# Performance work log

Hardware: AMD Instinct MI355X
Metric: run time of the kernel (lower is better)

Reference implementation:

```python
import jax, jax.numpy as jnp
import numpy as np

B, S = 32, 4096
HID, MEM, ATT = 512, 512, 512


def setup_inputs() -> dict:
    key = jax.random.key(0)
    k1, k2, k3, k4, k5, k6, k7 = jax.random.split(key, 7)
    scale_h = 1.0 / np.sqrt(HID)
    scale_m = 1.0 / np.sqrt(MEM)
    scale_a = 1.0 / np.sqrt(ATT)
    return {
        "hidden": jax.random.normal(k1, (B, HID), dtype=jnp.float32),
        "memory": jax.random.normal(k2, (B, S, MEM), dtype=jnp.float32),
        "mem_pad": jnp.zeros((B, S), dtype=jnp.bool_),
        "coverage": jax.random.uniform(k3, (B, S), dtype=jnp.float32),
        # params stored as (in, out) so x @ W == torch Linear(x)
        "W_h": jax.random.uniform(k4, (HID, ATT), minval=-scale_h, maxval=scale_h, dtype=jnp.float32),
        "W_m": jax.random.uniform(k5, (MEM, ATT), minval=-scale_m, maxval=scale_m, dtype=jnp.float32),
        "W_c": jax.random.uniform(k6, (ATT,), minval=-1.0, maxval=1.0, dtype=jnp.float32),
        "v": jax.random.uniform(k7, (ATT,), minval=-scale_a, maxval=scale_a, dtype=jnp.float32),
    }


def reference(hidden, memory, mem_pad, coverage, W_h, W_m, W_c, v):
    h = hidden @ W_h                                   # (B, A)
    m = jnp.einsum('bsd,da->bsa', memory, W_m)         # (B, S, A)
    c_feat = coverage[..., None] * W_c                 # (B, S, A) ; Linear(1->A) == scalar * weight row
    score = jnp.einsum('bsa,a->bs', jnp.tanh(h[:, None, :] + m + c_feat), v)  # (B, S)
    score = jnp.where(mem_pad, -jnp.inf, score)
    attn_weights = jax.nn.softmax(score, axis=-1)      # (B, S)
    context = jnp.einsum('bs,bsd->bd', attn_weights, memory)  # (B, D)
    return context, attn_weights
```

## Files before the change

### kernel.cpp

```cpp
#include <hip/hip_runtime.h>
#include <hip/hip_bf16.h>
#include <math.h>

#define BB 32
#define SS 4096
#define DMEM 512
#define DATT 512

typedef short short8 __attribute__((ext_vector_type(8)));
typedef float floatx4 __attribute__((ext_vector_type(4)));

__device__ inline short f2bf(float x) {
    unsigned u = __float_as_uint(x);
    unsigned r = (u + 0x7fffu + ((u >> 16) & 1u)) >> 16;
    return (short)(r & 0xffffu);
}

__device__ inline float fast_tanh(float x) {
    float e = __expf(2.0f * x);
    float r = __builtin_amdgcn_rcpf(e + 1.0f);
    return __builtin_fmaf(-2.0f, r, 1.0f);
}


__global__ void prep_wt_kernel(const float* __restrict__ Wm, short* __restrict__ Wt) {
    const int n0 = blockIdx.x * 32;
    const int k0 = blockIdx.y * 32;
    const int t = threadIdx.x;
    const int r = t >> 5, c = t & 31;
    __shared__ float lds[32 * 33];
#pragma unroll
    for (int j = 0; j < 4; ++j) {
        int kk = r + j * 8;
        lds[kk * 33 + c] = Wm[(size_t)(k0 + kk) * 512 + n0 + c];
    }
    __syncthreads();
#pragma unroll
    for (int j = 0; j < 4; ++j) {
        int nn = r + j * 8;
        Wt[(size_t)(n0 + nn) * 512 + k0 + c] = f2bf(lds[c * 33 + nn]);
    }
}

__global__ void prep_h_kernel(const float* __restrict__ hidden, const float* __restrict__ Wh,
                              float* __restrict__ h) {
    const int b = blockIdx.x;
    const int n = blockIdx.y * 256 + threadIdx.x;
    const int kc = blockIdx.z;
    float acc = 0.f;
#pragma unroll 8
    for (int k = kc * 128; k < kc * 128 + 128; ++k)
        acc += hidden[b * 512 + k] * Wh[(size_t)k * 512 + n];
    atomicAdd(&h[b * 512 + n], acc);
}


__global__ __launch_bounds__(1024, 4)
void fused_kernel(const float* __restrict__ memory,
                  const float* __restrict__ coverage,
                  const unsigned char* __restrict__ pad,
                  const short* __restrict__ Wt,
                  const float* __restrict__ h,
                  const float* __restrict__ Wc,
                  const float* __restrict__ v,
                  float* __restrict__ pOut,
                  float* __restrict__ mWS,
                  float* __restrict__ lWS,
                  float* __restrict__ ctxPart) {
    const int blk = blockIdx.x;
    const int b = blk >> 5;
    const int st = blk & 31;
    const int s0 = st * 128;

    const int tid = threadIdx.x;
    const int lane = tid & 63;
    const int wave = tid >> 6;
    const int wm = wave & 1;
    const int wn = wave >> 1;
    const int col = lane & 15;
    const int q = lane >> 4;

    __shared__ __align__(16) char smem[22024];
    char* bufA0 = smem;
    char* bufA1 = smem + 8192;
    float* covS   = (float*)(smem + 16384);
    float* sred   = (float*)(smem + 16896);
    float* scoreS = (float*)(smem + 20992);
    float* pS     = (float*)(smem + 21504);
    float* mlS    = (float*)(smem + 22016);
    float4* red4  = (float4*)smem;

    if (tid < 128) covS[tid] = coverage[(size_t)b * SS + s0 + tid];

    const float4* gA4 = (const float4*)(memory + ((size_t)b * SS + s0) * 512);
    const char* gB = (const char*)Wt;

    const int arow = tid >> 3, al8 = tid & 7;
    const int aoff = arow * 64 + (((al8 >> 1) ^ ((arow >> 1) & 3)) << 4) + ((al8 & 1) << 3);
    const int boff0 = (wn * 64 + col) * 1024 + q * 16;

    float4 apfA;

    floatx4 acc[4][4];
#pragma unroll
    for (int mi = 0; mi < 4; ++mi)
#pragma unroll
        for (int ni = 0; ni < 4; ++ni)
            acc[mi][ni] = (floatx4){0.f, 0.f, 0.f, 0.f};

    apfA = gA4[(size_t)arow * 128 + al8];
    {
        union { __hip_bfloat162 h2; unsigned u; } p0, p1;
        p0.h2 = __float22bfloat162_rn(make_float2(apfA.x, apfA.y));
        p1.h2 = __float22bfloat162_rn(make_float2(apfA.z, apfA.w));
        uint2 w; w.x = p0.u; w.y = p1.u;
        *(uint2*)(bufA0 + aoff) = w;
    }
    apfA = gA4[(size_t)arow * 128 + 8 + al8];
    asm volatile("s_waitcnt lgkmcnt(0)" ::: "memory");
    __builtin_amdgcn_sched_barrier(0);
    __builtin_amdgcn_s_barrier();

#pragma unroll
    for (int kt = 0; kt < 16; ++kt) {
        short8 bfc[4];
#pragma unroll
        for (int ni = 0; ni < 4; ++ni)
            bfc[ni] = *(const short8*)(gB + (size_t)(boff0 + ni * 16384) + kt * 64);

        if (kt < 15) {
            union { __hip_bfloat162 h2; unsigned u; } p0, p1;
            p0.h2 = __float22bfloat162_rn(make_float2(apfA.x, apfA.y));
            p1.h2 = __float22bfloat162_rn(make_float2(apfA.z, apfA.w));
            uint2 w; w.x = p0.u; w.y = p1.u;
            char* dst = ((kt + 1) & 1) ? bufA1 : bufA0;
            *(uint2*)(dst + aoff) = w;
            if (kt < 14)
                apfA = gA4[(size_t)arow * 128 + (kt + 2) * 8 + al8];
        }

        const char* abase = (kt & 1) ? bufA1 : bufA0;
        short8 af[4];
#pragma unroll
        for (int mi = 0; mi < 4; ++mi) {
            int row = wm * 64 + mi * 16 + col;
            af[mi] = *(const short8*)(abase + row * 64 + ((q ^ ((row >> 1) & 3)) << 4));
        }
#pragma unroll
        for (int mi = 0; mi < 4; ++mi)
#pragma unroll
            for (int ni = 0; ni < 4; ++ni)
                acc[mi][ni] = __builtin_amdgcn_mfma_f32_16x16x32_bf16(af[mi], bfc[ni], acc[mi][ni], 0, 0, 0);

        asm volatile("s_waitcnt lgkmcnt(0)" ::: "memory");
        __builtin_amdgcn_sched_barrier(0);
        __builtin_amdgcn_s_barrier();
    }

    __syncthreads();

    float hv[4], wcv[4], vv[4];
#pragma unroll
    for (int ni = 0; ni < 4; ++ni) {
        int n = wn * 64 + ni * 16 + col;
        hv[ni] = h[b * 512 + n];
        wcv[ni] = Wc[n];
        vv[ni] = v[n];
    }
    float rowAcc[4][4];
#pragma unroll
    for (int mi = 0; mi < 4; ++mi)
#pragma unroll
        for (int r = 0; r < 4; ++r)
            rowAcc[mi][r] = 0.f;
#pragma unroll
    for (int mi = 0; mi < 4; ++mi) {
#pragma unroll
        for (int r = 0; r < 4; ++r) {
            float cv = covS[wm * 64 + mi * 16 + q * 4 + r];
#pragma unroll
            for (int ni = 0; ni < 4; ++ni) {
                float val = acc[mi][ni][r] + hv[ni] + cv * wcv[ni];
                rowAcc[mi][r] += fast_tanh(val) * vv[ni];
            }
        }
    }
#pragma unroll
    for (int off = 1; off < 16; off <<= 1)
#pragma unroll
        for (int mi = 0; mi < 4; ++mi)
#pragma unroll
            for (int r = 0; r < 4; ++r)
                rowAcc[mi][r] += __shfl_xor(rowAcc[mi][r], off, 64);

    if (col == 0) {
#pragma unroll
        for (int mi = 0; mi < 4; ++mi)
#pragma unroll
            for (int r = 0; r < 4; ++r)
                sred[wn * 128 + wm * 64 + mi * 16 + q * 4 + r] = rowAcc[mi][r];
    }
    __syncthreads();

    if (tid < 128) {
        float sc = 0.f;
#pragma unroll
        for (int w = 0; w < 8; ++w) sc += sred[w * 128 + tid];
        if (pad[(size_t)b * SS + s0 + tid]) sc = -INFINITY;
        scoreS[tid] = sc;
    }
    __syncthreads();
    if (tid < 64) {
        float mx = fmaxf(scoreS[tid], scoreS[tid + 64]);
#pragma unroll
        for (int off = 32; off >= 1; off >>= 1) mx = fmaxf(mx, __shfl_xor(mx, off, 64));
        if (tid == 0) mlS[0] = mx;
    }
    __syncthreads();
    const float mtile = mlS[0];
    if (tid < 128) pS[tid] = __expf(scoreS[tid] - mtile);
    __syncthreads();
    if (tid < 64) {
        float sm = pS[tid] + pS[tid + 64];
#pragma unroll
        for (int off = 32; off >= 1; off >>= 1) sm += __shfl_xor(sm, off, 64);
        if (tid == 0) mlS[1] = sm;
    }
    __syncthreads();

    if (tid < 128) pOut[(size_t)b * SS + s0 + tid] = pS[tid];
    if (tid == 0) {
        mWS[b * 32 + st] = mtile;
        lWS[b * 32 + st] = mlS[1];
    }

    const int sg = tid >> 7;
    const int dc = tid & 127;
    const float4* m4 = (const float4*)(memory + ((size_t)b * SS + s0) * 512);
    float4 a4 = {0.f, 0.f, 0.f, 0.f};
#pragma unroll 8
    for (int i = 0; i < 16; ++i) {
        int s = sg * 16 + i;
        float w = pS[s];
        float4 f = m4[(size_t)s * 128 + dc];
        a4.x += w * f.x; a4.y += w * f.y; a4.z += w * f.z; a4.w += w * f.w;
    }
    red4[sg * 128 + dc] = a4;
    __syncthreads();
    if (tid < 128) {
        float4 o = {0.f, 0.f, 0.f, 0.f};
#pragma unroll
        for (int g2 = 0; g2 < 8; ++g2) {
            float4 r = red4[g2 * 128 + tid];
            o.x += r.x; o.y += r.y; o.z += r.z; o.w += r.w;
        }
        ((float4*)(ctxPart + ((size_t)(b * 32 + st)) * 512))[tid] = o;
    }
}

__global__ __launch_bounds__(512)
void combine_kernel(const float* __restrict__ mWS,
                    const float* __restrict__ lWS,
                    const float* __restrict__ ctxPart,
                    float* __restrict__ ctx,
                    float* __restrict__ attn) {
    const int b = blockIdx.x;
    const int tid = threadIdx.x;
    __shared__ float scaleS[32];
    __shared__ float gS[2];

    if (tid < 64) {
        float mv = (tid < 32) ? mWS[b * 32 + tid] : -INFINITY;
#pragma unroll
        for (int off = 32; off >= 1; off >>= 1) mv = fmaxf(mv, __shfl_xor(mv, off, 64));
        if (tid == 0) gS[0] = mv;
    }
    __syncthreads();
    const float gmax = gS[0];
    if (tid < 64) {
        float sc = 0.f, lv = 0.f;
        if (tid < 32) {
            sc = __expf(mWS[b * 32 + tid] - gmax);
            scaleS[tid] = sc;
            lv = lWS[b * 32 + tid] * sc;
        }
#pragma unroll
        for (int off = 32; off >= 1; off >>= 1) lv += __shfl_xor(lv, off, 64);
        if (tid == 0) gS[1] = lv;
    }
    __syncthreads();
    const float inv = 1.0f / gS[1];

    float facc = 0.f;
#pragma unroll 8
    for (int st = 0; st < 32; ++st)
        facc += ctxPart[((size_t)(b * 32 + st)) * 512 + tid] * scaleS[st];
    ctx[b * 512 + tid] = facc * inv;

#pragma unroll
    for (int j = 0; j < 8; ++j) {
        size_t idx = (size_t)b * SS + j * 512 + tid;
        attn[idx] = attn[idx] * scaleS[(j * 512 + tid) >> 7] * inv;
    }
}

extern "C" void kernel_launch(void* const* d_in, const int* in_sizes, int n_in,
                              void* d_out, int out_size, void* d_ws, size_t ws_size,
                              hipStream_t stream) {
    (void)in_sizes; (void)n_in; (void)out_size; (void)ws_size;
    const float* hidden   = (const float*)d_in[0];
    const float* memory   = (const float*)d_in[1];
    const unsigned char* mem_pad = (const unsigned char*)d_in[2];
    const float* coverage = (const float*)d_in[3];
    const float* Wh       = (const float*)d_in[4];
    const float* Wm       = (const float*)d_in[5];
    const float* Wc       = (const float*)d_in[6];
    const float* v        = (const float*)d_in[7];

    char* ws = (char*)d_ws;
    short* Wt      = (short*)ws;
    float* h       = (float*)(ws + 512 * 1024);
    float* mWS     = (float*)(ws + 576 * 1024);
    float* lWS     = (float*)(ws + 580 * 1024);
    float* ctxPart = (float*)(ws + 584 * 1024);

    float* ctx  = (float*)d_out;
    float* attn = (float*)d_out + BB * 512;

    hipMemsetAsync(h, 0, BB * 512 * sizeof(float), stream);
    prep_wt_kernel<<<dim3(16, 16), dim3(256), 0, stream>>>(Wm, Wt);
    prep_h_kernel<<<dim3(32, 2, 4), dim3(256), 0, stream>>>(hidden, Wh, h);
    fused_kernel<<<dim3(BB * 32), dim3(1024), 0, stream>>>(
        memory, coverage, mem_pad, Wt, h, Wc, v, attn, mWS, lWS, ctxPart);
    combine_kernel<<<dim3(BB), dim3(512), 0, stream>>>(mWS, lWS, ctxPart, ctx, attn);
}
```

Baseline: 517.0 us.

## Stage W_m bf16 tiles into LDS via async global_load_lds double buffering

```diff
diff --git a/kernel.cpp b/kernel.cpp
--- a/kernel.cpp
+++ b/kernel.cpp
@@ -20,6 +20,12 @@
     float e = __expf(2.0f * x);
     float r = __builtin_amdgcn_rcpf(e + 1.0f);
     return __builtin_fmaf(-2.0f, r, 1.0f);
+}
+
+__device__ inline void gld_lds16(const void* g, void* l) {
+    __builtin_amdgcn_global_load_lds(
+        (const __attribute__((address_space(1))) unsigned int*)g,
+        (__attribute__((address_space(3))) unsigned int*)l, 16, 0, 0);
 }
 
 
@@ -80,14 +86,16 @@
     const int col = lane & 15;
     const int q = lane >> 4;
 
-    __shared__ __align__(16) char smem[22024];
-    char* bufA0 = smem;
-    char* bufA1 = smem + 8192;
-    float* covS   = (float*)(smem + 16384);
-    float* sred   = (float*)(smem + 16896);
-    float* scoreS = (float*)(smem + 20992);
-    float* pS     = (float*)(smem + 21504);
-    float* mlS    = (float*)(smem + 22016);
+    __shared__ __align__(16) char smem[87560];
+    char* bufB0 = smem;
+    char* bufB1 = smem + 32768;
+    char* bufA0 = smem + 65536;
+    char* bufA1 = smem + 73728;
+    float* covS   = (float*)(smem + 81920);
+    float* sred   = (float*)(smem + 82432);
+    float* scoreS = (float*)(smem + 86528);
+    float* pS     = (float*)(smem + 87040);
+    float* mlS    = (float*)(smem + 87552);
     float4* red4  = (float4*)smem;
 
     if (tid < 128) covS[tid] = coverage[(size_t)b * SS + s0 + tid];
@@ -97,7 +105,6 @@
 
     const int arow = tid >> 3, al8 = tid & 7;
     const int aoff = arow * 64 + (((al8 >> 1) ^ ((arow >> 1) & 3)) << 4) + ((al8 & 1) << 3);
-    const int boff0 = (wn * 64 + col) * 1024 + q * 16;
 
     float4 apfA;
 
@@ -109,6 +116,16 @@
             acc[mi][ni] = (floatx4){0.f, 0.f, 0.f, 0.f};
 
     apfA = gA4[(size_t)arow * 128 + al8];
+    __builtin_amdgcn_sched_barrier(0);
+#pragma unroll
+    for (int it = 0; it < 2; ++it) {
+        int ci = it * 1024 + tid;
+        int row = ci >> 2;
+        int gch = (ci & 3) ^ ((row >> 1) & 3);
+        gld_lds16(gB + (size_t)row * 1024 + gch * 16,
+                  bufB0 + it * 16384 + wave * 1024);
+    }
+    __builtin_amdgcn_sched_barrier(0);
     {
         union { __hip_bfloat162 h2; unsigned u; } p0, p1;
         p0.h2 = __float22bfloat162_rn(make_float2(apfA.x, apfA.y));
@@ -116,17 +133,44 @@
         uint2 w; w.x = p0.u; w.y = p1.u;
         *(uint2*)(bufA0 + aoff) = w;
     }
+    __builtin_amdgcn_sched_barrier(0);
     apfA = gA4[(size_t)arow * 128 + 8 + al8];
+    __builtin_amdgcn_sched_barrier(0);
+    asm volatile("s_waitcnt vmcnt(1)" ::: "memory");
+    __builtin_amdgcn_sched_barrier(0);
     asm volatile("s_waitcnt lgkmcnt(0)" ::: "memory");
     __builtin_amdgcn_sched_barrier(0);
     __builtin_amdgcn_s_barrier();
+    __builtin_amdgcn_sched_barrier(0);
 
 #pragma unroll
     for (int kt = 0; kt < 16; ++kt) {
-        short8 bfc[4];
-#pragma unroll
-        for (int ni = 0; ni < 4; ++ni)
-            bfc[ni] = *(const short8*)(gB + (size_t)(boff0 + ni * 16384) + kt * 64);
+        if (kt < 15) {
+            char* ldsB = ((kt + 1) & 1) ? bufB1 : bufB0;
+#pragma unroll
+            for (int it = 0; it < 2; ++it) {
+                int ci = it * 1024 + tid;
+                int row = ci >> 2;
+                int gch = (ci & 3) ^ ((row >> 1) & 3);
+                gld_lds16(gB + (size_t)row * 1024 + (kt + 1) * 64 + gch * 16,
+                          ldsB + it * 16384 + wave * 1024);
+            }
+        }
+        __builtin_amdgcn_sched_barrier(0);
+
+        const char* abase = (kt & 1) ? bufA1 : bufA0;
+        const char* bbase = (kt & 1) ? bufB1 : bufB0;
+        short8 af[4], bf[4];
+#pragma unroll
+        for (int mi = 0; mi < 4; ++mi) {
+            int row = wm * 64 + mi * 16 + col;
+            af[mi] = *(const short8*)(abase + row * 64 + ((q ^ ((row >> 1) & 3)) << 4));
+        }
+#pragma unroll
+        for (int ni = 0; ni < 4; ++ni) {
+            int row = wn * 64 + ni * 16 + col;
+            bf[ni] = *(const short8*)(bbase + row * 64 + ((q ^ ((row >> 1) & 3)) << 4));
+        }
 
         if (kt < 15) {
             union { __hip_bfloat162 h2; unsigned u; } p0, p1;
@@ -138,23 +182,26 @@
             if (kt < 14)
                 apfA = gA4[(size_t)arow * 128 + (kt + 2) * 8 + al8];
         }
-
-        const char* abase = (kt & 1) ? bufA1 : bufA0;
-        short8 af[4];
-#pragma unroll
-        for (int mi = 0; mi < 4; ++mi) {
-            int row = wm * 64 + mi * 16 + col;
-            af[mi] = *(const short8*)(abase + row * 64 + ((q ^ ((row >> 1) & 3)) << 4));
-        }
+        __builtin_amdgcn_sched_barrier(0);
+
 #pragma unroll
         for (int mi = 0; mi < 4; ++mi)
 #pragma unroll
             for (int ni = 0; ni < 4; ++ni)
-                acc[mi][ni] = __builtin_amdgcn_mfma_f32_16x16x32_bf16(af[mi], bfc[ni], acc[mi][ni], 0, 0, 0);
-
-        asm volatile("s_waitcnt lgkmcnt(0)" ::: "memory");
-        __builtin_amdgcn_sched_barrier(0);
-        __builtin_amdgcn_s_barrier();
+                acc[mi][ni] = __builtin_amdgcn_mfma_f32_16x16x32_bf16(af[mi], bf[ni], acc[mi][ni], 0, 0, 0);
+
+        if (kt < 15) {
+            if (kt < 14) {
+                asm volatile("s_waitcnt vmcnt(1)" ::: "memory");
+            } else {
+                asm volatile("s_waitcnt vmcnt(0)" ::: "memory");
+            }
+            __builtin_amdgcn_sched_barrier(0);
+            asm volatile("s_waitcnt lgkmcnt(0)" ::: "memory");
+            __builtin_amdgcn_sched_barrier(0);
+            __builtin_amdgcn_s_barrier();
+            __builtin_amdgcn_sched_barrier(0);
+        }
     }
 
     __syncthreads();
```

New measurement: 455.9 us. -11.8%, faster.
